# Kernel tuning notes

Hardware: AMD Instinct MI355X
Metric: run time of the kernel (lower is better)

Reference implementation:

```python
import jax, jax.numpy as jnp
import numpy as np

DIM = 64; HEADS = 4; HD = DIM // HEADS; TOPK = 40; RS = 2  # region_size = max(4//t_patch,1)
B = 16; T = 2048; NR = T // RS
EPS = 1e-5
SCALE = DIM ** -0.5  # qk_scale=None -> self.dim**-0.5 (as in source, NOT head_dim)


def conv1d(x, w, pad, groups=1):
    return jax.lax.conv_general_dilated(x, w, (1,), [(pad, pad)],
        dimension_numbers=('NCH', 'OIH', 'NCH'), feature_group_count=groups)


def bn(x, g, b):
    # eval-mode BatchNorm1d with fresh running stats (mean=0, var=1)
    s = g * np.float32(1.0 / np.sqrt(1.0 + EPS))
    return x * s[None, :, None] + b[None, :, None]


def _blocks(t):
    # (B, C, T) -> (B, H, NR, RS, HD)
    return t.reshape(B, HEADS, HD, NR, RS).transpose(0, 1, 3, 4, 2)


def forward(x, n1_g, n1_b, wq, bnq_g, bnq_b, wk, bnk_g, bnk_b, wv,
            lepe_w, lepe_b, out_w, out_b, n2_g, n2_b,
            fc1_w, bn1_g, bn1_b, fr, fi, frb, fib, fc2_w, bn2_g, bn2_b):
    # ---------- Time_bra: top-k region routing attention ----------
    xn = bn(x, n1_g, n1_b)
    q = bn(conv1d(xn, wq, 1), bnq_g, bnq_b)
    k = bn(conv1d(xn, wk, 1), bnk_g, bnk_b)
    v = conv1d(xn, wv, 0)
    # region pooling on detached q/k (avg_pool1d, T divisible by RS)
    qd = jax.lax.stop_gradient(q); kd = jax.lax.stop_gradient(k)
    q_r = qd.reshape(B, DIM, NR, RS).mean(-1)
    k_r = kd.reshape(B, DIM, NR, RS).mean(-1)
    a_r = jnp.einsum('bcr,bcs->brs', q_r, k_r)          # (B, NR, NR) region affinity
    idx = jax.lax.top_k(a_r, TOPK)[1]                   # (B, NR, TOPK), shared across heads
    qb = _blocks(q); kb = _blocks(k); vb = _blocks(v)   # (B, H, NR, RS, HD)
    ie = idx[:, None, :, :, None, None]                 # (B, 1, NR, TOPK, 1, 1)
    kg = jnp.take_along_axis(kb[:, :, None], ie, axis=3).reshape(B, HEADS, NR, TOPK * RS, HD)
    vg = jnp.take_along_axis(vb[:, :, None], ie, axis=3).reshape(B, HEADS, NR, TOPK * RS, HD)
    logits = jnp.einsum('bhrqd,bhrkd->bhrqk', qb, kg) * jnp.float32(SCALE)
    attn = jax.nn.softmax(logits, axis=-1)
    o = jnp.einsum('bhrqk,bhrkd->bhrqd', attn, vg)      # (B, H, NR, RS, HD)
    o = o.transpose(0, 1, 4, 2, 3).reshape(B, DIM, T)
    o = o + conv1d(v, lepe_w, 1, groups=DIM) + lepe_b[None, :, None]  # lepe (depthwise)
    o = conv1d(o, out_w, 0) + out_b[None, :, None]
    x = x + o
    # ---------- Frequencydomain_FFN ----------
    yn = bn(x, n2_g, n2_b)
    h = jax.nn.relu(bn(conv1d(yn, fc1_w, 0), bn1_g, bn1_b))  # (B, 2C, T)
    h = h.transpose(0, 2, 1)                                  # (B, T, 2C)
    f = jnp.fft.fft(h, axis=1, norm='ortho')
    # torch.einsum('bnc,cc->bnc', x, r) contracts with diag(r) (repeated index)
    xr = jax.nn.relu(jnp.einsum('bnc,cc->bnc', f.real, fr) - jnp.einsum('bnc,cc->bnc', f.imag, fi) + frb)
    xi = jax.nn.relu(jnp.einsum('bnc,cc->bnc', f.imag, fr) + jnp.einsum('bnc,cc->bnc', f.real, fi) + fib)
    h = jnp.fft.ifft(jax.lax.complex(xr, xi), axis=1, norm='ortho').real.astype(jnp.float32)
    h = bn(conv1d(h.transpose(0, 2, 1), fc2_w, 0), bn2_g, bn2_b)
    return x + h


def setup_inputs() -> dict:
    ks = jax.random.split(jax.random.key(0), 16)
    C = DIM; C2 = 2 * DIM
    g = lambda i, shape, s: (s * jax.random.normal(ks[i], shape)).astype(jnp.float32)
    return {
        'x': jax.random.normal(ks[0], (B, C, T), dtype=jnp.float32),
        'n1_g': jnp.ones((C,), jnp.float32), 'n1_b': jnp.zeros((C,), jnp.float32),
        'wq': g(1, (C, C, 3), 0.05), 'bnq_g': jnp.ones((C,), jnp.float32), 'bnq_b': jnp.zeros((C,), jnp.float32),
        'wk': g(2, (C, C, 3), 0.05), 'bnk_g': jnp.ones((C,), jnp.float32), 'bnk_b': jnp.zeros((C,), jnp.float32),
        'wv': g(3, (C, C, 1), 0.05),
        'lepe_w': g(4, (C, 1, 3), 0.1), 'lepe_b': jnp.zeros((C,), jnp.float32),
        'out_w': g(5, (C, C, 1), 0.05), 'out_b': jnp.zeros((C,), jnp.float32),
        'n2_g': jnp.ones((C,), jnp.float32), 'n2_b': jnp.zeros((C,), jnp.float32),
        'fc1_w': g(6, (C2, C, 1), 0.05), 'bn1_g': jnp.ones((C2,), jnp.float32), 'bn1_b': jnp.zeros((C2,), jnp.float32),
        'fr': g(7, (C2, C2), 0.02), 'fi': g(8, (C2, C2), 0.02),
        'frb': g(9, (C2,), 0.02), 'fib': g(10, (C2,), 0.02),
        'fc2_w': g(11, (C, C2, 1), 0.05), 'bn2_g': jnp.ones((C,), jnp.float32), 'bn2_b': jnp.zeros((C,), jnp.float32),
    }


def reference(x, n1_g, n1_b, wq, bnq_g, bnq_b, wk, bnk_g, bnk_b, wv,
              lepe_w, lepe_b, out_w, out_b, n2_g, n2_b,
              fc1_w, bn1_g, bn1_b, fr, fi, frb, fib, fc2_w, bn2_g, bn2_b):
    return forward(x, n1_g, n1_b, wq, bnq_g, bnq_b, wk, bnk_g, bnk_b, wv,
                   lepe_w, lepe_b, out_w, out_b, n2_g, n2_b,
                   fc1_w, bn1_g, bn1_b, fr, fi, frb, fib, fc2_w, bn2_g, bn2_b)
```

## Files before the change

kernel.cpp:

```cpp
#include <hip/hip_runtime.h>
#include <hip/hip_bf16.h>

#define T 2048
#define NR 1024
#define TOPK 40

static __device__ __forceinline__ float bnscale() { return 0.9999950000374997f; }

__global__ __launch_bounds__(256) void k_qkv(
    const float* __restrict__ x, const float* __restrict__ n1_g, const float* __restrict__ n1_b,
    const float* __restrict__ wq, const float* __restrict__ bnq_g, const float* __restrict__ bnq_b,
    const float* __restrict__ wk, const float* __restrict__ bnk_g, const float* __restrict__ bnk_b,
    const float* __restrict__ wv,
    float* __restrict__ q_t, float* __restrict__ k_t, float* __restrict__ v_t,
    float* __restrict__ q_rc, float* __restrict__ k_rc)
{
  const int b = blockIdx.y;
  const int tile = blockIdx.x >> 2;
  const int oc0 = (blockIdx.x & 3) * 16;
  const int t0 = tile * 64;
  const int r0 = tile * 32;
  const int tid = threadIdx.x;
  const float INVS = bnscale();

  __shared__ float xn[64][67];
  __shared__ float ot[16][67];

  for (int i = tid; i < 64 * 66; i += 256) {
    int c = i / 66, tt = i - c * 66;
    int t = t0 + tt - 1;
    float v = (t >= 0 && t < T) ? x[(size_t)(b * 64 + c) * T + t] : 0.f;
    xn[c][tt] = v * (n1_g[c] * INVS) + n1_b[c];
  }
  __syncthreads();

  const int w = tid >> 6, lane = tid & 63;
  const int ob = oc0 + __builtin_amdgcn_readfirstlane(w) * 4;

  float accq[4], acck[4], accv[4];
#pragma unroll
  for (int j = 0; j < 4; ++j) { accq[j] = 0.f; acck[j] = 0.f; accv[j] = 0.f; }

#pragma unroll 1
  for (int c0 = 0; c0 < 64; c0 += 4) {
    float xr[4][3];
#pragma unroll
    for (int cc = 0; cc < 4; ++cc) {
      xr[cc][0] = xn[c0 + cc][lane];
      xr[cc][1] = xn[c0 + cc][lane + 1];
      xr[cc][2] = xn[c0 + cc][lane + 2];
    }
#pragma unroll
    for (int o4 = 0; o4 < 4; ++o4) {
      int o = ob + o4;
      const float* wqo = wq + o * 192 + c0 * 3;
      const float* wko = wk + o * 192 + c0 * 3;
      const float* wvo = wv + o * 64 + c0;
      float aq = accq[o4], ak = acck[o4], av = accv[o4];
#pragma unroll
      for (int cc = 0; cc < 4; ++cc) {
        aq += xr[cc][0] * wqo[cc * 3 + 0] + xr[cc][1] * wqo[cc * 3 + 1] + xr[cc][2] * wqo[cc * 3 + 2];
        ak += xr[cc][0] * wko[cc * 3 + 0] + xr[cc][1] * wko[cc * 3 + 1] + xr[cc][2] * wko[cc * 3 + 2];
        av += xr[cc][1] * wvo[cc];
      }
      accq[o4] = aq; acck[o4] = ak; accv[o4] = av;
    }
  }

#pragma unroll
  for (int o4 = 0; o4 < 4; ++o4) {
    int o = ob + o4;
    ot[o - oc0][lane] = accq[o4] * (bnq_g[o] * INVS) + bnq_b[o];
  }
  __syncthreads();
  for (int i = tid; i < 1024; i += 256) {
    int cl = i & 15, tt = i >> 4;
    q_t[((size_t)(b * T + t0 + tt)) * 64 + oc0 + cl] = ot[cl][tt];
  }
  for (int i = tid; i < 512; i += 256) {
    int rr = i & 31, cl = i >> 5;
    q_rc[((size_t)(b * 64 + oc0 + cl)) * NR + r0 + rr] = 0.5f * (ot[cl][2 * rr] + ot[cl][2 * rr + 1]);
  }
  __syncthreads();

#pragma unroll
  for (int o4 = 0; o4 < 4; ++o4) {
    int o = ob + o4;
    ot[o - oc0][lane] = acck[o4] * (bnk_g[o] * INVS) + bnk_b[o];
  }
  __syncthreads();
  for (int i = tid; i < 1024; i += 256) {
    int cl = i & 15, tt = i >> 4;
    k_t[((size_t)(b * T + t0 + tt)) * 64 + oc0 + cl] = ot[cl][tt];
  }
  for (int i = tid; i < 512; i += 256) {
    int rr = i & 31, cl = i >> 5;
    k_rc[((size_t)(b * 64 + oc0 + cl)) * NR + r0 + rr] = 0.5f * (ot[cl][2 * rr] + ot[cl][2 * rr + 1]);
  }
  __syncthreads();

#pragma unroll
  for (int o4 = 0; o4 < 4; ++o4) {
    ot[ob + o4 - oc0][lane] = accv[o4];
  }
  __syncthreads();
  for (int i = tid; i < 1024; i += 256) {
    int cl = i & 15, tt = i >> 4;
    v_t[((size_t)(b * T + t0 + tt)) * 64 + oc0 + cl] = ot[cl][tt];
  }
}

__global__ __launch_bounds__(256) void k_scores(
    const float* __restrict__ q_rc, const float* __restrict__ k_rc, int* __restrict__ sel)
{
  const int ib = blockIdx.x;
  const int xcd = ib & 7;
  const int slot = ib >> 3;
  const int b = xcd * 2 + (slot >> 6);
  const int r0 = (slot & 63) * 16;
  const int tid = threadIdx.x;
  const int w = tid >> 6, lane = tid & 63;

  __shared__ float qsT[16][68];

  for (int i = tid; i < 1024; i += 256) {
    int rr = i & 15, c = i >> 4;
    qsT[rr][c] = q_rc[((size_t)(b * 64 + c)) * NR + r0 + rr];
  }
  __syncthreads();

  const int row0 = w * 4;

  float4 acc[4][4];
#pragma unroll
  for (int r = 0; r < 4; ++r)
#pragma unroll
    for (int j = 0; j < 4; ++j) acc[r][j] = make_float4(0.f, 0.f, 0.f, 0.f);

  const float4* kp = (const float4*)(k_rc + ((size_t)b * 64) * NR);
#pragma unroll 1
  for (int c0 = 0; c0 < 64; c0 += 4) {
    float4 qv[4];
#pragma unroll
    for (int r = 0; r < 4; ++r) qv[r] = *(const float4*)&qsT[row0 + r][c0];
#pragma unroll
    for (int cc = 0; cc < 4; ++cc) {
      const float4* kr = kp + (size_t)(c0 + cc) * 256 + lane;
      float4 k0 = kr[0], k1 = kr[64], k2 = kr[128], k3 = kr[192];
      float qf[4] = { (&qv[0].x)[cc], (&qv[1].x)[cc], (&qv[2].x)[cc], (&qv[3].x)[cc] };
#pragma unroll
      for (int r = 0; r < 4; ++r) {
        float q = qf[r];
        acc[r][0].x += q * k0.x; acc[r][0].y += q * k0.y; acc[r][0].z += q * k0.z; acc[r][0].w += q * k0.w;
        acc[r][1].x += q * k1.x; acc[r][1].y += q * k1.y; acc[r][1].z += q * k1.z; acc[r][1].w += q * k1.w;
        acc[r][2].x += q * k2.x; acc[r][2].y += q * k2.y; acc[r][2].z += q * k2.z; acc[r][2].w += q * k2.w;
        acc[r][3].x += q * k3.x; acc[r][3].y += q * k3.y; acc[r][3].z += q * k3.z; acc[r][3].w += q * k3.w;
      }
    }
  }

  unsigned pk[4][16];
#pragma unroll
  for (int r = 0; r < 4; ++r) {
#pragma unroll
    for (int j = 0; j < 4; ++j) {
      const float* av = &acc[r][j].x;
#pragma unroll
      for (int s = 0; s < 4; ++s) {
        unsigned u = __float_as_uint(av[s]);
        u ^= (unsigned)((int)u >> 31) | 0x80000000u;
        int idx = 256 * j + 4 * lane + s;
        pk[r][4 * j + s] = (u & 0xFFFFFC00u) | (unsigned)(1023 - idx);
      }
    }
  }

  unsigned p[4] = {0u, 0u, 0u, 0u};
  unsigned thr[4];
  bool done[4] = {false, false, false, false};
#pragma unroll 1
  for (int bit = 31; bit >= 0; --bit) {
#pragma unroll
    for (int r = 0; r < 4; ++r) {
      if (done[r]) continue;
      unsigned X = p[r] | (1u << bit);
      int c = 0;
#pragma unroll
      for (int j = 0; j < 16; ++j)
        c += __popcll(__ballot(pk[r][j] >= X));
      if (c >= TOPK) p[r] = X;
      if (c == TOPK) { thr[r] = X; done[r] = true; }
    }
    if (done[0] && done[1] && done[2] && done[3]) break;
  }
#pragma unroll
  for (int r = 0; r < 4; ++r)
    if (!done[r]) thr[r] = p[r];

#pragma unroll
  for (int r = 0; r < 4; ++r) {
    const unsigned X = thr[r];
    int* srow = sel + ((size_t)(b * NR + r0 + row0 + r)) * TOPK;
    int base = 0;
#pragma unroll
    for (int j = 0; j < 16; ++j) {
      bool win = pk[r][j] >= X;
      unsigned long long m = __ballot(win);
      int before = __builtin_amdgcn_mbcnt_hi((unsigned)(m >> 32),
                   __builtin_amdgcn_mbcnt_lo((unsigned)m, 0));
      if (win) srow[base + before] = 1023 - (int)(pk[r][j] & 1023u);
      base += __popcll(m);
    }
  }
}

__global__ __launch_bounds__(256) void k_attn(
    const float* __restrict__ q_t, const float* __restrict__ k_t, const float* __restrict__ v_t,
    const int* __restrict__ sel, const float* __restrict__ lepe_w, const float* __restrict__ lepe_b,
    float* __restrict__ o_t)
{
  const int ib = blockIdx.x;
  const int xcd = ib & 7;
  const int slot = ib >> 3;
  const int b = xcd * 2 + (slot >> 10);
  const int r = slot & 1023;
  const int tid = threadIdx.x;

  __shared__ __align__(16) float kg[80][68];
  __shared__ __align__(16) float qb[2][64];
  __shared__ int   toff[80];
  __shared__ __align__(16) float lg[4][2][84];
  __shared__ float vl[4][64];

  float (*part)[2][64] = (float (*)[2][64])&kg[0][0];

  if (tid < 40) {
    int s = sel[((size_t)(b * NR + r)) * TOPK + tid];
    toff[2 * tid]     = s * 512;
    toff[2 * tid + 1] = s * 512 + 256;
  }
  if (tid >= 128 && tid < 256) {
    int i = tid - 128;
    int s = i >> 6, c = i & 63;
    qb[s][c] = q_t[((size_t)(b * T + r * 2 + s)) * 64 + c];
  }
  {
    int idx = tid >> 6, c = tid & 63;
    int t = 2 * r - 1 + idx;
    vl[idx][c] = (t >= 0 && t < T) ? v_t[((size_t)(b * T + t)) * 64 + c] : 0.f;
  }
  __syncthreads();

  {
    const char* kbase = (const char*)(k_t + (size_t)b * T * 64);
    for (int i = tid; i < 80 * 16; i += 256) {
      int row = i >> 4, c4 = i & 15;
      float4 kv = *(const float4*)(kbase + toff[row] + c4 * 16);
      *(float4*)&kg[row][c4 * 4] = kv;
    }
  }
  __syncthreads();

  const int h = tid >> 6, lane = tid & 63;

  {
    float4 q0[4], q1[4];
#pragma unroll
    for (int j = 0; j < 4; ++j) {
      q0[j] = *(const float4*)&qb[0][h * 16 + j * 4];
      q1[j] = *(const float4*)&qb[1][h * 16 + j * 4];
    }
    for (int col = lane; col < 80; col += 64) {
      float a0 = 0.f, a1 = 0.f;
#pragma unroll
      for (int j = 0; j < 4; ++j) {
        float4 kv = *(const float4*)&kg[col][h * 16 + j * 4];
        a0 += q0[j].x * kv.x + q0[j].y * kv.y + q0[j].z * kv.z + q0[j].w * kv.w;
        a1 += q1[j].x * kv.x + q1[j].y * kv.y + q1[j].z * kv.z + q1[j].w * kv.w;
      }
      lg[h][0][col] = a0 * 0.125f;
      lg[h][1][col] = a1 * 0.125f;
    }
  }

  for (int sq = 0; sq < 2; ++sq) {
    float a = lg[h][sq][lane];
    float bb = (lane < 16) ? lg[h][sq][64 + lane] : -INFINITY;
    float m = fmaxf(a, bb);
    for (int mm = 32; mm >= 1; mm >>= 1) m = fmaxf(m, __shfl_xor(m, mm));
    float ea = expf(a - m);
    float eb = (lane < 16) ? expf(bb - m) : 0.f;
    float ssum = ea + eb;
    for (int mm = 32; mm >= 1; mm >>= 1) ssum += __shfl_xor(ssum, mm);
    float inv = 1.f / ssum;
    lg[h][sq][lane] = ea * inv;
    if (lane < 16) lg[h][sq][64 + lane] = eb * inv;
  }
  __syncthreads();

  {
    const int c = tid & 63, j = tid >> 6;
    const int sq = j & 1, half = j >> 1;
    const int hh = c >> 4;
    const char* vbase = (const char*)(v_t + (size_t)b * T * 64) + c * 4;
    float acc = 0.f;
#pragma unroll 2
    for (int ch = 0; ch < 10; ++ch) {
      int col0 = half * 40 + ch * 4;
      float4 p = *(const float4*)&lg[hh][sq][col0];
      float v0 = *(const float*)(vbase + toff[col0 + 0]);
      float v1 = *(const float*)(vbase + toff[col0 + 1]);
      float v2 = *(const float*)(vbase + toff[col0 + 2]);
      float v3 = *(const float*)(vbase + toff[col0 + 3]);
      acc += p.x * v0 + p.y * v1 + p.z * v2 + p.w * v3;
    }
    part[half][sq][c] = acc;
  }
  __syncthreads();

  if (tid < 128) {
    int sq = tid >> 6, c = tid & 63;
    float o = part[0][sq][c] + part[1][sq][c];
    float lep = lepe_b[c];
#pragma unroll
    for (int kk = 0; kk < 3; ++kk) lep += lepe_w[c * 3 + kk] * vl[sq + kk][c];
    o_t[((size_t)(b * T + 2 * r + sq)) * 64 + c] = o + lep;
  }
}

__global__ __launch_bounds__(256) void k_mix(
    const float* __restrict__ x, const float* __restrict__ o_t,
    const float* __restrict__ out_w, const float* __restrict__ out_b,
    const float* __restrict__ n2_g, const float* __restrict__ n2_b,
    const float* __restrict__ fc1_w, const float* __restrict__ bn1_g, const float* __restrict__ bn1_b,
    float* __restrict__ xres, float* __restrict__ h_c)
{
  const int b = blockIdx.y;
  const int t0 = blockIdx.x * 16;
  const int tid = threadIdx.x;
  const float INVS = bnscale();

  __shared__ float ol[16][65];
  __shared__ float yn[16][65];
  __shared__ float xl[16][65];
  __shared__ float wo[64][65];
  __shared__ float w1[128][65];
  __shared__ float res2[128][17];

  for (int i = tid; i < 1024; i += 256) {
    int tt = i >> 6, c = i & 63;
    ol[tt][c] = o_t[((size_t)(b * T + t0 + tt)) * 64 + c];
  }
  for (int i = tid; i < 1024; i += 256) {
    int c = i >> 4, tt = i & 15;
    xl[tt][c] = x[(size_t)(b * 64 + c) * T + t0 + tt];
  }
  for (int i = tid; i < 4096; i += 256) {
    int c = i >> 6, cc = i & 63;
    wo[cc][c] = out_w[i];
  }
  for (int i = tid; i < 8192; i += 256) {
    int cc = i >> 6, c = i & 63;
    w1[cc][c] = fc1_w[i];
  }
  __syncthreads();

  {
    const int c = tid & 63, grp = tid >> 6;
    float a0 = out_b[c], a1 = a0, a2 = a0, a3 = a0;
    for (int cc = 0; cc < 64; ++cc) {
      float wv = wo[cc][c];
      a0 += wv * ol[grp * 4 + 0][cc];
      a1 += wv * ol[grp * 4 + 1][cc];
      a2 += wv * ol[grp * 4 + 2][cc];
      a3 += wv * ol[grp * 4 + 3][cc];
    }
    float g2 = n2_g[c] * INVS, b2 = n2_b[c];
    float av[4] = {a0, a1, a2, a3};
#pragma unroll
    for (int j = 0; j < 4; ++j) {
      int tt = grp * 4 + j;
      float xr = xl[tt][c] + av[j];
      xres[((size_t)(b * T + t0 + tt)) * 64 + c] = xr;
      yn[tt][c] = xr * g2 + b2;
    }
  }
  __syncthreads();

  {
    const int cc = tid & 127, half = tid >> 7;
    float acc[8];
#pragma unroll
    for (int j = 0; j < 8; ++j) acc[j] = 0.f;
    for (int c = 0; c < 64; ++c) {
      float wv = w1[cc][c];
#pragma unroll
      for (int j = 0; j < 8; ++j) acc[j] += wv * yn[half * 8 + j][c];
    }
    float g1 = bn1_g[cc] * INVS, b1 = bn1_b[cc];
#pragma unroll
    for (int j = 0; j < 8; ++j)
      res2[cc][half * 8 + j] = fmaxf(acc[j] * g1 + b1, 0.f);
  }
  __syncthreads();

  for (int i = tid; i < 2048; i += 256) {
    int tt = i & 15, cc = i >> 4;
    h_c[((size_t)(b * 128 + cc)) * T + t0 + tt] = res2[cc][tt];
  }
}

__global__ __launch_bounds__(256) void k_fft(
    const float* __restrict__ h_c, const float* __restrict__ fr, const float* __restrict__ fi,
    const float* __restrict__ frb, const float* __restrict__ fib, float* __restrict__ g_c)
{
  const int b = blockIdx.y;
  const int c2 = blockIdx.x;
  const int tid = threadIdx.x;

  __shared__ float re[2048];
  __shared__ float im[2048];
  __shared__ float twr[512];
  __shared__ float twi[512];

  for (int i = tid; i < 512; i += 256) {
    float ang = -6.283185307179586f * (float)i * (1.0f / 2048.0f);
    float sn, cs;
    sincosf(ang, &sn, &cs);
    twr[i] = cs; twi[i] = sn;
  }
  const float* hrow = h_c + ((size_t)(b * 128 + c2)) * T;
  for (int t = tid; t < 2048; t += 256) {
    re[t] = hrow[t];
    im[t] = 0.f;
  }
  __syncthreads();

#pragma unroll
  for (int m = 2048; m >= 8; m >>= 2) {
    const int q = m >> 2;
    const int f = 2048 / m;
#pragma unroll
    for (int k = tid; k < 512; k += 256) {
      int p = k & (q - 1);
      int g = k / q;
      int i0 = g * m + p, i1 = i0 + q, i2 = i0 + 2 * q, i3 = i0 + 3 * q;
      float a0r = re[i0], a0i = im[i0], a1r = re[i1], a1i = im[i1];
      float a2r = re[i2], a2i = im[i2], a3r = re[i3], a3i = im[i3];
      float s0r = a0r + a2r, s0i = a0i + a2i;
      float s1r = a0r - a2r, s1i = a0i - a2i;
      float s2r = a1r + a3r, s2i = a1i + a3i;
      float s3r = a1r - a3r, s3i = a1i - a3i;
      re[i0] = s0r + s2r; im[i0] = s0i + s2i;
      float y1r = s1r + s3i, y1i = s1i - s3r;
      float y2r = s0r - s2r, y2i = s0i - s2i;
      float y3r = s1r - s3i, y3i = s1i + s3r;
      float w1r = twr[f * p], w1i = twi[f * p];
      float w2r = w1r * w1r - w1i * w1i, w2i = 2.f * w1r * w1i;
      float w3r = w2r * w1r - w2i * w1i, w3i = w2r * w1i + w2i * w1r;
      re[i1] = y1r * w1r - y1i * w1i; im[i1] = y1r * w1i + y1i * w1r;
      re[i2] = y2r * w2r - y2i * w2i; im[i2] = y2r * w2i + y2i * w2r;
      re[i3] = y3r * w3r - y3i * w3i; im[i3] = y3r * w3i + y3i * w3r;
    }
    __syncthreads();
  }
  for (int k = tid; k < 1024; k += 256) {
    int i0 = 2 * k, i1 = 2 * k + 1;
    float ur = re[i0], ui = im[i0], vr = re[i1], vi = im[i1];
    re[i0] = ur + vr; im[i0] = ui + vi;
    re[i1] = ur - vr; im[i1] = ui - vi;
  }
  __syncthreads();

  const float SC = 0.022097086912079608f;
  const float fa = fr[c2 * 129];
  const float fb = fi[c2 * 129];
  const float fra = frb[c2];
  const float fia = fib[c2];
  for (int t = tid; t < 2048; t += 256) {
    float rr = re[t] * SC, ii = im[t] * SC;
    re[t] = fmaxf(rr * fa - ii * fb + fra, 0.f);
    im[t] = fmaxf(ii * fa + rr * fb + fia, 0.f);
  }
  __syncthreads();

  for (int k = tid; k < 1024; k += 256) {
    int i0 = 2 * k, i1 = 2 * k + 1;
    float ur = re[i0], ui = im[i0], vr = re[i1], vi = im[i1];
    re[i0] = ur + vr; im[i0] = ui + vi;
    re[i1] = ur - vr; im[i1] = ui - vi;
  }
  __syncthreads();
#pragma unroll
  for (int m = 8; m <= 2048; m <<= 2) {
    const int q = m >> 2;
    const int f = 2048 / m;
#pragma unroll
    for (int k = tid; k < 512; k += 256) {
      int p = k & (q - 1);
      int g = k / q;
      int i0 = g * m + p, i1 = i0 + q, i2 = i0 + 2 * q, i3 = i0 + 3 * q;
      float y0r = re[i0], y0i = im[i0];
      float b1r = re[i1], b1i = im[i1];
      float b2r = re[i2], b2i = im[i2];
      float b3r = re[i3], b3i = im[i3];
      float w1r = twr[f * p], w1i = twi[f * p];
      float w2r = w1r * w1r - w1i * w1i, w2i = 2.f * w1r * w1i;
      float w3r = w2r * w1r - w2i * w1i, w3i = w2r * w1i + w2i * w1r;
      float z1r = b1r * w1r + b1i * w1i, z1i = b1i * w1r - b1r * w1i;
      float z2r = b2r * w2r + b2i * w2i, z2i = b2i * w2r - b2r * w2i;
      float z3r = b3r * w3r + b3i * w3i, z3i = b3i * w3r - b3r * w3i;
      float u0r = y0r + z2r, u0i = y0i + z2i;
      float u2r = y0r - z2r, u2i = y0i - z2i;
      float u1r = z1r + z3r, u1i = z1i + z3i;
      float dr = z1r - z3r, di = z1i - z3i;
      float u3r = -di, u3i = dr;
      re[i0] = u0r + u1r; im[i0] = u0i + u1i;
      re[i2] = u0r - u1r; im[i2] = u0i - u1i;
      re[i1] = u2r + u3r; im[i1] = u2i + u3i;
      re[i3] = u2r - u3r; im[i3] = u2i - u3i;
    }
    __syncthreads();
  }

  float* grow = g_c + ((size_t)(b * 128 + c2)) * T;
  for (int t = tid; t < 2048; t += 256)
    grow[t] = re[t] * SC;
}

__global__ __launch_bounds__(256) void k_out(
    const float* __restrict__ g_c, const float* __restrict__ xres,
    const float* __restrict__ fc2_w, const float* __restrict__ bn2_g, const float* __restrict__ bn2_b,
    float* __restrict__ out)
{
  const int b = blockIdx.y;
  const int t0 = blockIdx.x * 16;
  const int tid = threadIdx.x;
  const float INVS = bnscale();

  __shared__ float gl[16][129];
  __shared__ float w2[128][65];
  __shared__ float res[64][17];

  for (int i = tid; i < 2048; i += 256) {
    int tt = i & 15, cc = i >> 4;
    gl[tt][cc] = g_c[((size_t)(b * 128 + cc)) * T + t0 + tt];
  }
  for (int i = tid; i < 8192; i += 256) {
    int c = i >> 7, cc = i & 127;
    w2[cc][c] = fc2_w[i];
  }
  __syncthreads();

  {
    const int c = tid & 63, grp = tid >> 6;
    float a0 = 0.f, a1 = 0.f, a2 = 0.f, a3 = 0.f;
    for (int cc = 0; cc < 128; ++cc) {
      float wv = w2[cc][c];
      a0 += wv * gl[grp * 4 + 0][cc];
      a1 += wv * gl[grp * 4 + 1][cc];
      a2 += wv * gl[grp * 4 + 2][cc];
      a3 += wv * gl[grp * 4 + 3][cc];
    }
    float g2 = bn2_g[c] * INVS, b2 = bn2_b[c];
    float av[4] = {a0, a1, a2, a3};
#pragma unroll
    for (int j = 0; j < 4; ++j) {
      int tt = grp * 4 + j;
      res[c][tt] = xres[((size_t)(b * T + t0 + tt)) * 64 + c] + av[j] * g2 + b2;
    }
  }
  __syncthreads();

  for (int i = tid; i < 1024; i += 256) {
    int tt = i & 15, c = i >> 4;
    out[(size_t)(b * 64 + c) * T + t0 + tt] = res[c][tt];
  }
}

extern "C" void kernel_launch(void* const* d_in, const int* in_sizes, int n_in,
                              void* d_out, int out_size, void* d_ws, size_t ws_size,
                              hipStream_t stream) {
  (void)in_sizes; (void)n_in; (void)out_size; (void)ws_size;
  const float* x     = (const float*)d_in[0];
  const float* n1_g  = (const float*)d_in[1];
  const float* n1_b  = (const float*)d_in[2];
  const float* wq    = (const float*)d_in[3];
  const float* bnq_g = (const float*)d_in[4];
  const float* bnq_b = (const float*)d_in[5];
  const float* wk    = (const float*)d_in[6];
  const float* bnk_g = (const float*)d_in[7];
  const float* bnk_b = (const float*)d_in[8];
  const float* wv    = (const float*)d_in[9];
  const float* lepe_w= (const float*)d_in[10];
  const float* lepe_b= (const float*)d_in[11];
  const float* out_w = (const float*)d_in[12];
  const float* out_b = (const float*)d_in[13];
  const float* n2_g  = (const float*)d_in[14];
  const float* n2_b  = (const float*)d_in[15];
  const float* fc1_w = (const float*)d_in[16];
  const float* bn1_g = (const float*)d_in[17];
  const float* bn1_b = (const float*)d_in[18];
  const float* fr    = (const float*)d_in[19];
  const float* fi    = (const float*)d_in[20];
  const float* frb   = (const float*)d_in[21];
  const float* fib   = (const float*)d_in[22];
  const float* fc2_w = (const float*)d_in[23];
  const float* bn2_g = (const float*)d_in[24];
  const float* bn2_b = (const float*)d_in[25];

  float* out = (float*)d_out;
  float* ws  = (float*)d_ws;
  const size_t M1 = (size_t)1 << 20;

  float* q_t  = ws;
  float* k_t  = ws + 2 * M1;
  float* v_t  = ws + 4 * M1;
  float* q_rc = ws + 6 * M1;
  float* k_rc = ws + 7 * M1;
  float* o_t  = ws + 8 * M1;
  float* xrs  = ws + 10 * M1;
  int*   sel  = (int*)(ws + 12 * M1);
  float* h_c  = ws;
  float* g_c  = ws + 4 * M1;

  k_qkv<<<dim3(128, 16), 256, 0, stream>>>(x, n1_g, n1_b, wq, bnq_g, bnq_b,
                                           wk, bnk_g, bnk_b, wv, q_t, k_t, v_t, q_rc, k_rc);
  k_scores<<<dim3(1024), 256, 0, stream>>>(q_rc, k_rc, sel);
  k_attn<<<dim3(16384), 256, 0, stream>>>(q_t, k_t, v_t, sel, lepe_w, lepe_b, o_t);
  k_mix<<<dim3(128, 16), 256, 0, stream>>>(x, o_t, out_w, out_b, n2_g, n2_b,
                                           fc1_w, bn1_g, bn1_b, xrs, h_c);
  k_fft<<<dim3(128, 16), 256, 0, stream>>>(h_c, fr, fi, frb, fib, g_c);
  k_out<<<dim3(128, 16), 256, 0, stream>>>(g_c, xrs, fc2_w, bn2_g, bn2_b, out);
}
```

Baseline: 417.2 us.

## Split score columns across waves with per-wave top-k and shared-memory merge

In k_scores, each wave now computes all 16 query rows against its own 256-column slice of k_rc, rather than 4 rows against all 1024 columns. This cuts the redundant k_rc reads each wave performs, and the k loads are double-buffered to overlap with the FMAs. Each wave runs a ballot radix select to keep its own top-40 per row and writes them to shared memory. A rank-counting merge over the 160 candidates then produces the final top-40. The trade-off is extra LDS, a barrier and a merge pass. Selected indices are now written in descending-score order instead of index order.

```diff
diff --git a/kernel.cpp b/kernel.cpp
--- a/kernel.cpp
+++ b/kernel.cpp
@@ -122,6 +122,7 @@
   const int w = tid >> 6, lane = tid & 63;
 
   __shared__ float qsT[16][68];
+  __shared__ unsigned list[16][160];
 
   for (int i = tid; i < 1024; i += 256) {
     int rr = i & 15, c = i >> 4;
@@ -129,88 +130,116 @@
   }
   __syncthreads();
 
-  const int row0 = w * 4;
-
-  float4 acc[4][4];
-#pragma unroll
-  for (int r = 0; r < 4; ++r)
-#pragma unroll
-    for (int j = 0; j < 4; ++j) acc[r][j] = make_float4(0.f, 0.f, 0.f, 0.f);
-
-  const float4* kp = (const float4*)(k_rc + ((size_t)b * 64) * NR);
+  const float4* kp4 = (const float4*)(k_rc + ((size_t)b * 64) * NR);
+  const int coff = w * 64 + lane;
+
+  float4 acc[16];
+#pragma unroll
+  for (int r = 0; r < 16; ++r) acc[r] = make_float4(0.f, 0.f, 0.f, 0.f);
+
+  float4 kA[4], kB[4];
+#pragma unroll
+  for (int u = 0; u < 4; ++u) kA[u] = kp4[(size_t)u * 256 + coff];
+
 #pragma unroll 1
-  for (int c0 = 0; c0 < 64; c0 += 4) {
-    float4 qv[4];
-#pragma unroll
-    for (int r = 0; r < 4; ++r) qv[r] = *(const float4*)&qsT[row0 + r][c0];
-#pragma unroll
-    for (int cc = 0; cc < 4; ++cc) {
-      const float4* kr = kp + (size_t)(c0 + cc) * 256 + lane;
-      float4 k0 = kr[0], k1 = kr[64], k2 = kr[128], k3 = kr[192];
-      float qf[4] = { (&qv[0].x)[cc], (&qv[1].x)[cc], (&qv[2].x)[cc], (&qv[3].x)[cc] };
-#pragma unroll
-      for (int r = 0; r < 4; ++r) {
-        float q = qf[r];
-        acc[r][0].x += q * k0.x; acc[r][0].y += q * k0.y; acc[r][0].z += q * k0.z; acc[r][0].w += q * k0.w;
-        acc[r][1].x += q * k1.x; acc[r][1].y += q * k1.y; acc[r][1].z += q * k1.z; acc[r][1].w += q * k1.w;
-        acc[r][2].x += q * k2.x; acc[r][2].y += q * k2.y; acc[r][2].z += q * k2.z; acc[r][2].w += q * k2.w;
-        acc[r][3].x += q * k3.x; acc[r][3].y += q * k3.y; acc[r][3].z += q * k3.z; acc[r][3].w += q * k3.w;
+  for (int ch = 0; ch < 16; ch += 2) {
+#pragma unroll
+    for (int u = 0; u < 4; ++u) kB[u] = kp4[(size_t)((ch + 1) * 4 + u) * 256 + coff];
+    {
+      const int c0 = ch * 4;
+#pragma unroll
+      for (int r = 0; r < 16; ++r) {
+        float4 qv = *(const float4*)&qsT[r][c0];
+        acc[r].x += qv.x * kA[0].x + qv.y * kA[1].x + qv.z * kA[2].x + qv.w * kA[3].x;
+        acc[r].y += qv.x * kA[0].y + qv.y * kA[1].y + qv.z * kA[2].y + qv.w * kA[3].y;
+        acc[r].z += qv.x * kA[0].z + qv.y * kA[1].z + qv.z * kA[2].z + qv.w * kA[3].z;
+        acc[r].w += qv.x * kA[0].w + qv.y * kA[1].w + qv.z * kA[2].w + qv.w * kA[3].w;
       }
     }
-  }
-
-  unsigned pk[4][16];
-#pragma unroll
-  for (int r = 0; r < 4; ++r) {
-#pragma unroll
-    for (int j = 0; j < 4; ++j) {
-      const float* av = &acc[r][j].x;
-#pragma unroll
-      for (int s = 0; s < 4; ++s) {
-        unsigned u = __float_as_uint(av[s]);
-        u ^= (unsigned)((int)u >> 31) | 0x80000000u;
-        int idx = 256 * j + 4 * lane + s;
-        pk[r][4 * j + s] = (u & 0xFFFFFC00u) | (unsigned)(1023 - idx);
+    if (ch + 2 < 16) {
+#pragma unroll
+      for (int u = 0; u < 4; ++u) kA[u] = kp4[(size_t)((ch + 2) * 4 + u) * 256 + coff];
+    }
+    {
+      const int c0 = (ch + 1) * 4;
+#pragma unroll
+      for (int r = 0; r < 16; ++r) {
+        float4 qv = *(const float4*)&qsT[r][c0];
+        acc[r].x += qv.x * kB[0].x + qv.y * kB[1].x + qv.z * kB[2].x + qv.w * kB[3].x;
+        acc[r].y += qv.x * kB[0].y + qv.y * kB[1].y + qv.z * kB[2].y + qv.w * kB[3].y;
+        acc[r].z += qv.x * kB[0].z + qv.y * kB[1].z + qv.z * kB[2].z + qv.w * kB[3].z;
+        acc[r].w += qv.x * kB[0].w + qv.y * kB[1].w + qv.z * kB[2].w + qv.w * kB[3].w;
       }
     }
   }
 
-  unsigned p[4] = {0u, 0u, 0u, 0u};
-  unsigned thr[4];
-  bool done[4] = {false, false, false, false};
+  unsigned pk[16][4];
+#pragma unroll
+  for (int r = 0; r < 16; ++r) {
+    const float* av = &acc[r].x;
+#pragma unroll
+    for (int s = 0; s < 4; ++s) {
+      unsigned u = __float_as_uint(av[s]);
+      u ^= (unsigned)((int)u >> 31) | 0x80000000u;
+      int idx = 256 * w + 4 * lane + s;
+      pk[r][s] = (u & 0xFFFFFC00u) | (unsigned)(1023 - idx);
+    }
+  }
+
+  unsigned p[16];
+#pragma unroll
+  for (int r = 0; r < 16; ++r) p[r] = 0u;
+  unsigned doneMask = 0;
 #pragma unroll 1
   for (int bit = 31; bit >= 0; --bit) {
 #pragma unroll
-    for (int r = 0; r < 4; ++r) {
-      if (done[r]) continue;
+    for (int r = 0; r < 16; ++r) {
+      if (doneMask & (1u << r)) continue;
       unsigned X = p[r] | (1u << bit);
       int c = 0;
 #pragma unroll
-      for (int j = 0; j < 16; ++j)
+      for (int j = 0; j < 4; ++j)
         c += __popcll(__ballot(pk[r][j] >= X));
       if (c >= TOPK) p[r] = X;
-      if (c == TOPK) { thr[r] = X; done[r] = true; }
-    }
-    if (done[0] && done[1] && done[2] && done[3]) break;
-  }
-#pragma unroll
-  for (int r = 0; r < 4; ++r)
-    if (!done[r]) thr[r] = p[r];
-
-#pragma unroll
-  for (int r = 0; r < 4; ++r) {
-    const unsigned X = thr[r];
-    int* srow = sel + ((size_t)(b * NR + r0 + row0 + r)) * TOPK;
+      if (c == TOPK) doneMask |= (1u << r);
+    }
+    if (doneMask == 0xFFFFu) break;
+  }
+
+#pragma unroll
+  for (int r = 0; r < 16; ++r) {
+    const unsigned X = p[r];
     int base = 0;
 #pragma unroll
-    for (int j = 0; j < 16; ++j) {
+    for (int j = 0; j < 4; ++j) {
       bool win = pk[r][j] >= X;
       unsigned long long m = __ballot(win);
       int before = __builtin_amdgcn_mbcnt_hi((unsigned)(m >> 32),
                    __builtin_amdgcn_mbcnt_lo((unsigned)m, 0));
-      if (win) srow[base + before] = 1023 - (int)(pk[r][j] & 1023u);
+      if (win) list[r][w * 40 + base + before] = pk[r][j];
       base += __popcll(m);
     }
+  }
+  __syncthreads();
+
+#pragma unroll
+  for (int rr = 0; rr < 4; ++rr) {
+    const int r = w * 4 + rr;
+    unsigned v0 = list[r][lane];
+    unsigned v1 = list[r][lane + 64];
+    unsigned v2 = (lane < 32) ? list[r][lane + 128] : 0u;
+    int g0 = 0, g1 = 0, g2 = 0;
+#pragma unroll 4
+    for (int i = 0; i < 160; ++i) {
+      unsigned u = list[r][i];
+      g0 += (u > v0) ? 1 : 0;
+      g1 += (u > v1) ? 1 : 0;
+      g2 += (u > v2) ? 1 : 0;
+    }
+    int* srow = sel + ((size_t)(b * NR + r0 + r)) * TOPK;
+    if (g0 < TOPK) srow[g0] = 1023 - (int)(v0 & 1023u);
+    if (g1 < TOPK) srow[g1] = 1023 - (int)(v1 & 1023u);
+    if (lane < 32 && g2 < TOPK) srow[g2] = 1023 - (int)(v2 & 1023u);
   }
 }
 
```

Result: slower. 446.5 us (+7.0%).
